# Kernel tuning notes

Measured on AMD Instinct MI355X. Metric: run time of the kernel, lower is better.

Reference implementation:

```python
import jax, jax.numpy as jnp
from jax import lax
import numpy as np

CHUNK = 64      # chunk_size init kwarg
MAX_LOG = 20.0  # clamp bound used in ssd()
DT_BIAS = 0.01
NEG_SLOPE = 0.01  # torch LeakyReLU default


def segsum(a):
    """a: (..., T) -> (..., T, T); ss[i,j] = sum_{k=j+1..i} a[k], -inf above diag."""
    T = a.shape[-1]
    rep = jnp.broadcast_to(a[..., :, None], a.shape + (T,))
    strict_lower = jnp.tril(jnp.ones((T, T), dtype=bool), -1)
    ss = jnp.cumsum(jnp.where(strict_lower, rep, 0.0), axis=-2)
    keep = jnp.tril(jnp.ones((T, T), dtype=bool), 0)
    return jnp.where(keep, ss, -jnp.inf)


def setup_inputs() -> dict:
    key = jax.random.key(0)
    ks = jax.random.split(key, 7)
    T, B, S, F = 4096, 4, 16, 64   # time, batch, spatial heads, in_channels
    N, P, K = 16, 64, 5            # state_dim, head_dim, conv_size
    CH = 2 * N + P + 1             # bc_conv out channels = 97
    return {
        "x": jax.random.normal(ks[0], (T, B, S, F), dtype=jnp.float32),
        "conv_w": jax.random.normal(ks[1], (CH, F, K), dtype=jnp.float32) * 0.05,
        "conv_b": jax.random.normal(ks[2], (CH,), dtype=jnp.float32) * 0.05,
        "pass_w": jax.random.normal(ks[3], (1, F), dtype=jnp.float32) * 0.1,
        "pass_b": jax.random.normal(ks[4], (1,), dtype=jnp.float32) * 0.1,
        "red_w": jax.random.normal(ks[5], (1, P), dtype=jnp.float32) * 0.1,
        "red_b": jax.random.normal(ks[6], (1,), dtype=jnp.float32) * 0.1,
        "dt_param": jnp.zeros((1,), dtype=jnp.float32),  # torch init [0.0]
    }


def _forward(x, conv_w, conv_b, pass_w, pass_b, red_w, red_b, dt_param):
    T, B, S, F = x.shape
    CH, _, K = conv_w.shape
    P = red_w.shape[1]
    N = (CH - P - 1) // 2
    c = T // CHUNK

    # ---- _compute_ssm_params (parallel mode, causal left-pad) ----
    xr = jnp.moveaxis(x.reshape(T, B * S, F), 0, 2)          # (bs, F, T)
    xp = jnp.pad(xr, ((0, 0), (0, 0), (K - 1, 0)))           # left pad context
    bcax = lax.conv_general_dilated(
        xp, conv_w, window_strides=(1,), padding="VALID",
        dimension_numbers=("NCH", "OIH", "NCH")) + conv_b[None, :, None]
    bcax = jax.nn.sigmoid(bcax) + bcax                        # (bs, CH, T)
    bcax = bcax.reshape(B, S, CH, T)
    Bm = bcax[:, :, :N, :]                                    # (b,s,n,t)
    Cm = bcax[:, :, N:2 * N, :]                               # (b,s,n,t)
    A = -jnp.abs(bcax[:, :, 2 * N, :])                        # (b,s,t)
    Xc = bcax[:, :, 2 * N + 1:, :]                            # (b,s,p,t)
    dt = jax.nn.softplus(dt_param)[0] + DT_BIAS
    lAd = dt * A                                              # (b,s,t)
    Bd = Bm * ((jnp.exp(lAd) - 1.0) / (A + 1e-9))[:, :, None, :]
    Dx = x @ pass_w[0] + pass_b[0]                            # (t,b,s) passthrough

    # ---- ssd: chunked Mamba-2 scan ----
    Xb = jnp.moveaxis(Xc, 3, 0).swapaxes(0, 1).reshape(B, c, CHUNK, S, P)
    Bb = jnp.moveaxis(Bd, 3, 0).swapaxes(0, 1).reshape(B, c, CHUNK, S, N)
    Cb = jnp.moveaxis(Cm, 3, 0).swapaxes(0, 1).reshape(B, c, CHUNK, S, N)
    Ab = lAd.reshape(B, S, c, CHUNK)                          # (b,s,c,l)
    A_cumsum = jnp.cumsum(Ab, axis=-1)                        # (b,s,c,l)

    L = jnp.exp(jnp.clip(segsum(Ab), -MAX_LOG, MAX_LOG))      # (b,s,c,l,l)
    Y_diag = jnp.einsum("bclsn,bcmsn,bsclm,bcmsp->bclsp", Cb, Bb, L, Xb)

    decay_states = jnp.exp(jnp.clip(A_cumsum[..., -1:] - A_cumsum, -MAX_LOG, MAX_LOG))
    states = jnp.einsum("bclsn,bscl,bclsp->bcspn", Bb, decay_states, Xb)
    states = jnp.concatenate([jnp.zeros_like(states[:, :1]), states], axis=1)

    A_last = jnp.pad(A_cumsum[..., -1], ((0, 0), (0, 0), (1, 0)))  # (b,s,c+1)
    decay_chunk = jnp.exp(jnp.clip(segsum(A_last), -MAX_LOG, MAX_LOG))
    new_states = jnp.einsum("bszc,bcspn->bzspn", decay_chunk, states)
    states_c = new_states[:, :-1]                             # (b,c,s,p,n)

    state_decay_out = jnp.exp(A_cumsum)                       # (b,s,c,l), no clamp (as in source)
    Y_off = jnp.einsum("bclsn,bcspn,bscl->bclsp", Cb, states_c, state_decay_out)

    Y = (Y_diag + Y_off).reshape(B, T, S, P).swapaxes(0, 1)   # (t,b,s,p)

    # ---- reduce + leaky-relu passthrough ----
    y = Y @ red_w[0] + red_b[0]                               # (t,b,s)
    return y + jnp.where(Dx >= 0, Dx, NEG_SLOPE * Dx)


def reference(x, conv_w, conv_b, pass_w, pass_b, red_w, red_b, dt_param):
    return _forward(x, conv_w, conv_b, pass_w, pass_b, red_w, red_b, dt_param)
```

## Files before the change

kernel.cpp:

```cpp
#include <hip/hip_runtime.h>
#include <hip/hip_bf16.h>
#include <math.h>


#define Tn 4096
#define BSn 64
#define Fn 64
#define CHn 97
#define CHP 112
#define Kn 5
#define Nn 16
#define NCn 64

typedef __attribute__((ext_vector_type(8))) short bf16x8;
typedef __attribute__((ext_vector_type(4))) float f32x4;

static __device__ __forceinline__ unsigned short f2bf(float v) {
    __hip_bfloat16 b = __float2bfloat16(v);
    return *reinterpret_cast<unsigned short*>(&b);
}
static __device__ __forceinline__ float bf2f(unsigned short u) {
    unsigned v = ((unsigned)u) << 16;
    return __builtin_bit_cast(float, v);
}

#define OFF_BD   0
#define OFF_CM   (OFF_BD + 4194304)
#define OFF_LAD  (OFF_CM + 4194304)
#define OFF_XQ   (OFF_LAD + 262144)
#define OFF_DL   (OFF_XQ + 262144)
#define OFF_ACS  (OFF_DL + 262144)
#define OFF_SRED (OFF_ACS + 262144)
#define OFF_CSUM (OFF_SRED + 65536)
#define OFF_SNS  (OFF_CSUM + 4096)
#define OFF_WBH  (OFF_SNS + 65536)
#define OFF_WBL  (OFF_WBH + 17920)

__global__ __launch_bounds__(256) void k_prep(const float* __restrict__ conv_w,
                                              const float* __restrict__ pass_w,
                                              unsigned short* __restrict__ wbh,
                                              unsigned short* __restrict__ wbl) {
    int idx = blockIdx.x * 256 + threadIdx.x;
    if (idx >= Kn * CHP * Fn) return;
    int f = idx & 63;
    int rest = idx >> 6;
    int ch = rest % CHP;
    int k = rest / CHP;
    float w = 0.f;
    if (ch < CHn) w = conv_w[(ch * Fn + f) * Kn + k];
    else if (ch == 97 && k == 4) w = pass_w[f];
    unsigned short hi = f2bf(w);
    wbh[idx] = hi;
    if (ch >= 32 && ch < 48)
        wbl[(k * 16 + (ch - 32)) * 64 + f] = f2bf(w - bf2f(hi));
}

__global__ __launch_bounds__(256) void k_fwd(
    const float* __restrict__ x, const unsigned short* __restrict__ wbh,
    const unsigned short* __restrict__ wbl,
    const float* __restrict__ conv_b, const float* __restrict__ pass_b,
    const float* __restrict__ red_w, const float* __restrict__ red_b,
    const float* __restrict__ dtp,
    float* __restrict__ Cm_t, float* __restrict__ Acs_ws,
    float* __restrict__ yp_ws, float* __restrict__ sred_ws,
    float* __restrict__ csum_ws) {
    const int wgid = blockIdx.x;
    const int seq = wgid >> 3;
    const int bs = seq & 63;
    const int ci = ((seq >> 6) << 3) | (wgid & 7);
    const int tid = threadIdx.x;
    const int wv = tid >> 6, lane = tid & 63;
    const int qd = lane >> 4, n = lane & 15;

    __shared__ alignas(16) unsigned char pool[19584];
    unsigned short* xsb = (unsigned short*)pool;
    unsigned short* xlo = (unsigned short*)(pool + 9792);
    float* B0  = (float*)pool;
    float* Ct  = (float*)(pool + 5120);
    float* pxl = (float*)(pool + 10240);
    float* px2 = (float*)(pool + 11264);
    float* zsh = (float*)(pool + 12288);
    float* dl  = (float*)(pool + 12544);

    const int tB = (wv == 3) ? 6 : wv + 4;
    const unsigned short* pBw = (wv == 2) ? wbl : wbh;
    const int sB = (wv == 2) ? 16 : CHP;
    const int cB = (wv == 2) ? 0 : 16 * tB;
    bf16x8 wA[10], wB[10];
#pragma unroll
    for (int s = 0; s < 10; ++s) {
        const int k = s >> 1, f0 = 32 * (s & 1) + qd * 8;
        wA[s] = *(const bf16x8*)&wbh[((k * CHP + 16 * wv + n) << 6) + f0];
        wB[s] = *(const bf16x8*)&pBw[((k * sB + cB + n) << 6) + f0];
    }

    float4 v[5];
#pragma unroll
    for (int it = 0; it < 5; ++it) {
        int idx = tid + it * 256;
        int tt = idx >> 4, fq = (idx & 15) * 4;
        int t = ci * 64 - 4 + tt;
        v[it] = (idx < 68 * 16 && t >= 0)
                    ? *(const float4*)&x[(t * 64 + bs) * 64 + fq]
                    : make_float4(0.f, 0.f, 0.f, 0.f);
    }
#pragma unroll
    for (int it = 0; it < 5; ++it) {
        int idx = tid + it * 256;
        if (idx < 68 * 16) {
            int tt = idx >> 4, fq = (idx & 15) * 4;
            ushort4 h, lo;
            h.x = f2bf(v[it].x); lo.x = f2bf(v[it].x - bf2f(h.x));
            h.y = f2bf(v[it].y); lo.y = f2bf(v[it].y - bf2f(h.y));
            h.z = f2bf(v[it].z); lo.z = f2bf(v[it].z - bf2f(h.z));
            h.w = f2bf(v[it].w); lo.w = f2bf(v[it].w - bf2f(h.w));
            *(ushort4*)&xsb[tt * 72 + fq] = h;
            *(ushort4*)&xlo[tt * 72 + fq] = lo;
        }
    }
    __syncthreads();

    f32x4 accA[4], accB[4];
#pragma unroll
    for (int rg = 0; rg < 4; ++rg) {
        accA[rg] = (f32x4){0.f, 0.f, 0.f, 0.f};
        accB[rg] = (f32x4){0.f, 0.f, 0.f, 0.f};
    }
    if (wv == 2) {
#pragma unroll
        for (int s = 0; s < 10; ++s) {
            const int k = s >> 1, f0 = 32 * (s & 1) + qd * 8;
#pragma unroll
            for (int rg = 0; rg < 4; ++rg) {
                bf16x8 av = *(const bf16x8*)&xsb[(16 * rg + n + k) * 72 + f0];
                bf16x8 al = *(const bf16x8*)&xlo[(16 * rg + n + k) * 72 + f0];
                accA[rg] = __builtin_amdgcn_mfma_f32_16x16x32_bf16(av, wA[s], accA[rg], 0, 0, 0);
                accA[rg] = __builtin_amdgcn_mfma_f32_16x16x32_bf16(al, wA[s], accA[rg], 0, 0, 0);
                accA[rg] = __builtin_amdgcn_mfma_f32_16x16x32_bf16(av, wB[s], accA[rg], 0, 0, 0);
            }
        }
    } else {
#pragma unroll
        for (int s = 0; s < 10; ++s) {
            const int k = s >> 1, f0 = 32 * (s & 1) + qd * 8;
#pragma unroll
            for (int rg = 0; rg < 4; ++rg) {
                bf16x8 av = *(const bf16x8*)&xsb[(16 * rg + n + k) * 72 + f0];
                accA[rg] = __builtin_amdgcn_mfma_f32_16x16x32_bf16(av, wA[s], accA[rg], 0, 0, 0);
                accB[rg] = __builtin_amdgcn_mfma_f32_16x16x32_bf16(av, wB[s], accB[rg], 0, 0, 0);
            }
        }
    }
    __syncthreads();

    const int cbase = (bs * 64 + ci) * 64;
    float px[4][4];
#pragma unroll
    for (int rg = 0; rg < 4; ++rg)
#pragma unroll
        for (int reg = 0; reg < 4; ++reg) px[rg][reg] = 0.f;

    if (wv == 0) {
        const float cb0 = conv_b[n];
        const float cb4 = conv_b[64 + n], rw4 = red_w[31 + n];
#pragma unroll
        for (int rg = 0; rg < 4; ++rg)
#pragma unroll
            for (int reg = 0; reg < 4; ++reg) {
                int row = 16 * rg + 4 * qd + reg;
                float z0 = accA[rg][reg] + cb0;
                float a0 = z0 + 1.f / (1.f + __expf(-z0));
                accA[rg][reg] = a0;
                B0[row * 20 + n] = a0;
                float z4 = accB[rg][reg] + cb4;
                px[rg][reg] = (z4 + 1.f / (1.f + __expf(-z4))) * rw4;
            }
    } else if (wv == 1) {
        const float cb1 = conv_b[16 + n];
        const float cb5 = conv_b[80 + n], rw5 = red_w[47 + n];
#pragma unroll
        for (int rg = 0; rg < 4; ++rg)
#pragma unroll
            for (int reg = 0; reg < 4; ++reg) {
                int row = 16 * rg + 4 * qd + reg;
                float z1 = accA[rg][reg] + cb1;
                float a1 = z1 + 1.f / (1.f + __expf(-z1));
                Ct[row * 20 + n] = a1;
                Cm_t[(cbase + row) * 16 + n] = a1;
                float z5 = accB[rg][reg] + cb5;
                px[rg][reg] = (z5 + 1.f / (1.f + __expf(-z5))) * rw5;
            }
    } else if (wv == 2) {
        const float cb2 = conv_b[32 + n];
        const float rw2 = (n >= 1) ? red_w[n - 1] : 0.f;
#pragma unroll
        for (int rg = 0; rg < 4; ++rg)
#pragma unroll
            for (int reg = 0; reg < 4; ++reg) {
                int row = 16 * rg + 4 * qd + reg;
                if (n == 0) zsh[row] = accA[rg][reg];
                float z = accA[rg][reg] + cb2;
                px[rg][reg] = (z + 1.f / (1.f + __expf(-z))) * rw2;
            }
    } else {
        const float cb3 = conv_b[48 + n], rw3 = red_w[15 + n];
        const float cb6 = conv_b[96], rw6 = red_w[63];
        const float pb = pass_b[0], rb = red_b[0];
#pragma unroll
        for (int rg = 0; rg < 4; ++rg)
#pragma unroll
            for (int reg = 0; reg < 4; ++reg) {
                int row = 16 * rg + 4 * qd + reg;
                float z3 = accA[rg][reg] + cb3;
                px[rg][reg] = (z3 + 1.f / (1.f + __expf(-z3))) * rw3;
                if (n == 0) {
                    float z6 = accB[rg][reg] + cb6;
                    px[rg][reg] += (z6 + 1.f / (1.f + __expf(-z6))) * rw6;
                }
                if (n == 1) {
                    float Dx = accB[rg][reg] + pb;
                    float DL = (Dx >= 0.f) ? Dx : 0.01f * Dx;
                    dl[row] = DL + rb;
                }
            }
    }
#pragma unroll
    for (int m = 1; m < 16; m <<= 1)
#pragma unroll
        for (int rg = 0; rg < 4; ++rg)
#pragma unroll
            for (int reg = 0; reg < 4; ++reg)
                px[rg][reg] += __shfl_xor(px[rg][reg], m, 64);
    if (n == 0)
#pragma unroll
        for (int rg = 0; rg < 4; ++rg)
#pragma unroll
            for (int reg = 0; reg < 4; ++reg)
                pxl[wv * 64 + 16 * rg + 4 * qd + reg] = px[rg][reg];
    __syncthreads();

    const int l = lane;
    const float dt = log1pf(expf(dtp[0])) + 0.01f;
    float zA = zsh[l] + conv_b[32];
    float aA = zA + 1.f / (1.f + __expf(-zA));
    float An = -fabsf(aA);
    float lAd = dt * An;
    float fac = (__expf(lAd) - 1.f) / (An + 1e-9f);
    float s = lAd;
#pragma unroll
    for (int k = 1; k < 64; k <<= 1) {
        float t = __shfl_up(s, k, 64);
        if (l >= k) s += t;
    }
    const float acs_l = s;
    const float tot = __shfl(s, 63, 64);
    float xq = pxl[0 * 64 + l] + pxl[1 * 64 + l] + pxl[2 * 64 + l] + pxl[3 * 64 + l];
    const float wd = fac * xq;
    const float wsd = wd * __expf(fmaxf(tot - acs_l, -20.f));
    if (wv == 3) {
        Acs_ws[bs * Tn + ci * 64 + l] = acs_l;
        if (l == 0) csum_ws[bs * 64 + ci] = tot;
    }

    const float4 cc0 = *(const float4*)&Ct[l * 20 + 0];
    const float4 cc1 = *(const float4*)&Ct[l * 20 + 4];
    const float4 cc2 = *(const float4*)&Ct[l * 20 + 8];
    const float4 cc3 = *(const float4*)&Ct[l * 20 + 12];
    float part = 0.f;
#pragma unroll
    for (int mm = 0; mm < 16; ++mm) {
        const int m = 16 * wv + mm;
        const float4 b0 = *(const float4*)&B0[m * 20 + 0];
        const float4 b1 = *(const float4*)&B0[m * 20 + 4];
        const float4 b2 = *(const float4*)&B0[m * 20 + 8];
        const float4 b3 = *(const float4*)&B0[m * 20 + 12];
        float g = cc0.x * b0.x + cc0.y * b0.y + cc0.z * b0.z + cc0.w * b0.w +
                  cc1.x * b1.x + cc1.y * b1.y + cc1.z * b1.z + cc1.w * b1.w +
                  cc2.x * b2.x + cc2.y * b2.y + cc2.z * b2.z + cc2.w * b2.w +
                  cc3.x * b3.x + cc3.y * b3.y + cc3.z * b3.z + cc3.w * b3.w;
        float am = __shfl(acs_l, m, 64);
        float wm = __shfl(wd, m, 64);
        float arg = (m <= l) ? fmaxf(acs_l - am, -20.f) : -20.f;
        part += __expf(arg) * g * wm;
    }
    px2[wv * 64 + l] = part;

    if (wv == 0) {
        float sp = 0.f;
#pragma unroll
        for (int rg = 0; rg < 4; ++rg)
#pragma unroll
            for (int reg = 0; reg < 4; ++reg)
                sp += accA[rg][reg] * __shfl(wsd, 16 * rg + 4 * qd + reg, 64);
        sp += __shfl_xor(sp, 16, 64);
        sp += __shfl_xor(sp, 32, 64);
        if (l < 16) sred_ws[(bs * 64 + ci) * 16 + l] = sp;
    }
    __syncthreads();

    if (wv == 0)
        yp_ws[bs * Tn + ci * 64 + l] =
            px2[0 * 64 + l] + px2[1 * 64 + l] + px2[2 * 64 + l] + px2[3 * 64 + l] + dl[l];
}

__global__ __launch_bounds__(256) void k_out(
    const float* __restrict__ Cm_t, const float* __restrict__ Acs_ws,
    const float* __restrict__ sred_ws, const float* __restrict__ csum_ws,
    const float* __restrict__ yp_ws, float* __restrict__ out) {
    const int bs = blockIdx.y;
    const int tid = threadIdx.x;
    const int wv = tid >> 6, l = tid & 63;
    const int ci = blockIdx.x * 4 + wv;
    __shared__ float sn[4][16];
    const int base = bs * Tn + ci * 64;

    const float dexp = __expf(csum_ws[bs * 64 + l]);
#pragma unroll
    for (int j = 0; j < 4; ++j) {
        const int n = 4 * wv + j;
        float s = sred_ws[(bs * 64 + l) * 16 + n];
        float d = dexp;
#pragma unroll
        for (int k = 1; k < 64; k <<= 1) {
            float dp = __shfl_up(d, k, 64);
            float sp = __shfl_up(s, k, 64);
            if (l >= k) {
                s = d * sp + s;
                d = d * dp;
            }
        }
        float se = __shfl_up(s, 1, 64);
        float sns = (l == 0) ? 0.f : se;
        if ((l >> 2) == blockIdx.x) sn[l & 3][n] = sns;
    }

    const float4* crow = (const float4*)&Cm_t[((bs * 64 + ci) * 64 + l) * 16];
    float4 c0 = crow[0], c1 = crow[1], c2 = crow[2], c3 = crow[3];
    float yp = yp_ws[base + l];
    float acl = Acs_ws[base + l];
    __syncthreads();

    const float* s = sn[wv];
    float go = c0.x * s[0] + c0.y * s[1] + c0.z * s[2] + c0.w * s[3] +
               c1.x * s[4] + c1.y * s[5] + c1.z * s[6] + c1.w * s[7] +
               c2.x * s[8] + c2.y * s[9] + c2.z * s[10] + c2.w * s[11] +
               c3.x * s[12] + c3.y * s[13] + c3.z * s[14] + c3.w * s[15];
    out[(ci * 64 + l) * 64 + bs] = yp + __expf(acl) * go;
}

extern "C" void kernel_launch(void* const* d_in, const int* in_sizes, int n_in,
                              void* d_out, int out_size, void* d_ws,
                              size_t ws_size, hipStream_t stream) {
    const float* x = (const float*)d_in[0];
    const float* conv_w = (const float*)d_in[1];
    const float* conv_b = (const float*)d_in[2];
    const float* pass_w = (const float*)d_in[3];
    const float* pass_b = (const float*)d_in[4];
    const float* red_w = (const float*)d_in[5];
    const float* red_b = (const float*)d_in[6];
    const float* dtp = (const float*)d_in[7];
    float* out = (float*)d_out;
    float* W = (float*)d_ws;
    (void)in_sizes; (void)n_in; (void)out_size; (void)ws_size;

    float* Cm_t = W + OFF_CM;
    float* yp_ws = W + OFF_DL;
    float* Acs_ws = W + OFF_ACS;
    float* sred_ws = W + OFF_SRED;
    float* csum_ws = W + OFF_CSUM;
    unsigned short* wbh = (unsigned short*)(W + OFF_WBH);
    unsigned short* wbl = (unsigned short*)(W + OFF_WBL);

    k_prep<<<dim3((Kn * CHP * Fn + 255) / 256), dim3(256), 0, stream>>>(
        conv_w, pass_w, wbh, wbl);
    k_fwd<<<dim3(NCn * BSn), dim3(256), 0, stream>>>(
        x, wbh, wbl, conv_b, pass_b, red_w, red_b, dtp,
        Cm_t, Acs_ws, yp_ws, sred_ws, csum_ws);
    k_out<<<dim3(NCn / 4, BSn), dim3(256), 0, stream>>>(
        Cm_t, Acs_ws, sred_ws, csum_ws, yp_ws, out);
}
```

Baseline: 202.0 us.

## Fuse inter-chunk state scan into forward kernel via decoupled look-back chain

Removes the separate k_out kernel. Each workgroup now takes a ticket from an atomic counter so chunks are processed in order, then waits on a per-sequence flag for the previous chunk's carried state. It combines that state with its own, publishes the result, and writes the final output directly. This drops the workspace round-trips for Cm, Acs, yp and sred and one kernel launch. In exchange it adds a serial dependency chain of 64 chunks per sequence, with spin-wait latency on each link.

```diff
diff --git a/kernel.cpp b/kernel.cpp
--- a/kernel.cpp
+++ b/kernel.cpp
@@ -25,6 +25,9 @@
 }
 
 #define OFF_BD   0
+#define OFF_CHS  OFF_BD
+#define OFF_FLG  (OFF_BD + 65536)
+#define OFF_TKT  (OFF_BD + 69888)
 #define OFF_CM   (OFF_BD + 4194304)
 #define OFF_LAD  (OFF_CM + 4194304)
 #define OFF_XQ   (OFF_LAD + 262144)
@@ -39,8 +42,12 @@
 __global__ __launch_bounds__(256) void k_prep(const float* __restrict__ conv_w,
                                               const float* __restrict__ pass_w,
                                               unsigned short* __restrict__ wbh,
-                                              unsigned short* __restrict__ wbl) {
+                                              unsigned short* __restrict__ wbl,
+                                              int* __restrict__ flags,
+                                              int* __restrict__ ticket) {
     int idx = blockIdx.x * 256 + threadIdx.x;
+    if (idx < NCn * BSn) flags[idx] = 0;
+    if (idx == NCn * BSn) *ticket = 0;
     if (idx >= Kn * CHP * Fn) return;
     int f = idx & 63;
     int rest = idx >> 6;
@@ -61,13 +68,8 @@
     const float* __restrict__ conv_b, const float* __restrict__ pass_b,
     const float* __restrict__ red_w, const float* __restrict__ red_b,
     const float* __restrict__ dtp,
-    float* __restrict__ Cm_t, float* __restrict__ Acs_ws,
-    float* __restrict__ yp_ws, float* __restrict__ sred_ws,
-    float* __restrict__ csum_ws) {
-    const int wgid = blockIdx.x;
-    const int seq = wgid >> 3;
-    const int bs = seq & 63;
-    const int ci = ((seq >> 6) << 3) | (wgid & 7);
+    float* __restrict__ Schain, int* __restrict__ flags,
+    int* __restrict__ ticket, float* __restrict__ out) {
     const int tid = threadIdx.x;
     const int wv = tid >> 6, lane = tid & 63;
     const int qd = lane >> 4, n = lane & 15;
@@ -81,6 +83,12 @@
     float* px2 = (float*)(pool + 11264);
     float* zsh = (float*)(pool + 12288);
     float* dl  = (float*)(pool + 12544);
+    float* sn  = (float*)(pool + 12800);
+    __shared__ int tkt_s;
+
+    if (tid == 0) tkt_s = atomicAdd(ticket, 1);
+    __syncthreads();
+    const int bs = tkt_s & 63, ci = tkt_s >> 6;
 
     const int tB = (wv == 3) ? 6 : wv + 4;
     const unsigned short* pBw = (wv == 2) ? wbl : wbh;
@@ -153,7 +161,6 @@
     }
     __syncthreads();
 
-    const int cbase = (bs * 64 + ci) * 64;
     float px[4][4];
 #pragma unroll
     for (int rg = 0; rg < 4; ++rg)
@@ -184,9 +191,7 @@
             for (int reg = 0; reg < 4; ++reg) {
                 int row = 16 * rg + 4 * qd + reg;
                 float z1 = accA[rg][reg] + cb1;
-                float a1 = z1 + 1.f / (1.f + __expf(-z1));
-                Ct[row * 20 + n] = a1;
-                Cm_t[(cbase + row) * 16 + n] = a1;
+                Ct[row * 20 + n] = z1 + 1.f / (1.f + __expf(-z1));
                 float z5 = accB[rg][reg] + cb5;
                 px[rg][reg] = (z5 + 1.f / (1.f + __expf(-z5))) * rw5;
             }
@@ -249,17 +254,51 @@
     float s = lAd;
 #pragma unroll
     for (int k = 1; k < 64; k <<= 1) {
-        float t = __shfl_up(s, k, 64);
-        if (l >= k) s += t;
+        float t2 = __shfl_up(s, k, 64);
+        if (l >= k) s += t2;
     }
     const float acs_l = s;
     const float tot = __shfl(s, 63, 64);
     float xq = pxl[0 * 64 + l] + pxl[1 * 64 + l] + pxl[2 * 64 + l] + pxl[3 * 64 + l];
     const float wd = fac * xq;
     const float wsd = wd * __expf(fmaxf(tot - acs_l, -20.f));
-    if (wv == 3) {
-        Acs_ws[bs * Tn + ci * 64 + l] = acs_l;
-        if (l == 0) csum_ws[bs * 64 + ci] = tot;
+
+    if (wv == 0) {
+        float sp = 0.f;
+#pragma unroll
+        for (int rg = 0; rg < 4; ++rg)
+#pragma unroll
+            for (int reg = 0; reg < 4; ++reg)
+                sp += accA[rg][reg] * __shfl(wsd, 16 * rg + 4 * qd + reg, 64);
+        sp += __shfl_xor(sp, 16, 64);
+        sp += __shfl_xor(sp, 32, 64);
+        if (lane < 16) {
+            const float dloc = __expf(tot);
+            float nprev = 0.f;
+            if (ci > 0) {
+                int* fp = &flags[bs * 64 + (ci - 1)];
+                long spin = 0;
+                while (__hip_atomic_load(fp, __ATOMIC_ACQUIRE,
+                                         __HIP_MEMORY_SCOPE_AGENT) == 0) {
+                    __builtin_amdgcn_s_sleep(2);
+                    if (++spin > 100000000L) break;
+                }
+                nprev = __hip_atomic_load(
+                    &Schain[(bs * 64 + (ci - 1)) * 16 + lane],
+                    __ATOMIC_RELAXED, __HIP_MEMORY_SCOPE_AGENT);
+            }
+            sn[lane] = nprev;
+            if (ci < NCn - 1) {
+                __hip_atomic_store(&Schain[(bs * 64 + ci) * 16 + lane],
+                                   dloc * nprev + sp, __ATOMIC_RELAXED,
+                                   __HIP_MEMORY_SCOPE_AGENT);
+                __builtin_amdgcn_s_waitcnt(0);
+                if (lane == 0)
+                    __hip_atomic_store(&flags[bs * 64 + ci], 1,
+                                       __ATOMIC_RELEASE,
+                                       __HIP_MEMORY_SCOPE_AGENT);
+            }
+        }
     }
 
     const float4 cc0 = *(const float4*)&Ct[l * 20 + 0];
@@ -284,68 +323,17 @@
         part += __expf(arg) * g * wm;
     }
     px2[wv * 64 + l] = part;
+    __syncthreads();
 
     if (wv == 0) {
-        float sp = 0.f;
-#pragma unroll
-        for (int rg = 0; rg < 4; ++rg)
-#pragma unroll
-            for (int reg = 0; reg < 4; ++reg)
-                sp += accA[rg][reg] * __shfl(wsd, 16 * rg + 4 * qd + reg, 64);
-        sp += __shfl_xor(sp, 16, 64);
-        sp += __shfl_xor(sp, 32, 64);
-        if (l < 16) sred_ws[(bs * 64 + ci) * 16 + l] = sp;
-    }
-    __syncthreads();
-
-    if (wv == 0)
-        yp_ws[bs * Tn + ci * 64 + l] =
-            px2[0 * 64 + l] + px2[1 * 64 + l] + px2[2 * 64 + l] + px2[3 * 64 + l] + dl[l];
-}
-
-__global__ __launch_bounds__(256) void k_out(
-    const float* __restrict__ Cm_t, const float* __restrict__ Acs_ws,
-    const float* __restrict__ sred_ws, const float* __restrict__ csum_ws,
-    const float* __restrict__ yp_ws, float* __restrict__ out) {
-    const int bs = blockIdx.y;
-    const int tid = threadIdx.x;
-    const int wv = tid >> 6, l = tid & 63;
-    const int ci = blockIdx.x * 4 + wv;
-    __shared__ float sn[4][16];
-    const int base = bs * Tn + ci * 64;
-
-    const float dexp = __expf(csum_ws[bs * 64 + l]);
-#pragma unroll
-    for (int j = 0; j < 4; ++j) {
-        const int n = 4 * wv + j;
-        float s = sred_ws[(bs * 64 + l) * 16 + n];
-        float d = dexp;
-#pragma unroll
-        for (int k = 1; k < 64; k <<= 1) {
-            float dp = __shfl_up(d, k, 64);
-            float sp = __shfl_up(s, k, 64);
-            if (l >= k) {
-                s = d * sp + s;
-                d = d * dp;
-            }
-        }
-        float se = __shfl_up(s, 1, 64);
-        float sns = (l == 0) ? 0.f : se;
-        if ((l >> 2) == blockIdx.x) sn[l & 3][n] = sns;
-    }
-
-    const float4* crow = (const float4*)&Cm_t[((bs * 64 + ci) * 64 + l) * 16];
-    float4 c0 = crow[0], c1 = crow[1], c2 = crow[2], c3 = crow[3];
-    float yp = yp_ws[base + l];
-    float acl = Acs_ws[base + l];
-    __syncthreads();
-
-    const float* s = sn[wv];
-    float go = c0.x * s[0] + c0.y * s[1] + c0.z * s[2] + c0.w * s[3] +
-               c1.x * s[4] + c1.y * s[5] + c1.z * s[6] + c1.w * s[7] +
-               c2.x * s[8] + c2.y * s[9] + c2.z * s[10] + c2.w * s[11] +
-               c3.x * s[12] + c3.y * s[13] + c3.z * s[14] + c3.w * s[15];
-    out[(ci * 64 + l) * 64 + bs] = yp + __expf(acl) * go;
+        float go = cc0.x * sn[0] + cc0.y * sn[1] + cc0.z * sn[2] + cc0.w * sn[3] +
+                   cc1.x * sn[4] + cc1.y * sn[5] + cc1.z * sn[6] + cc1.w * sn[7] +
+                   cc2.x * sn[8] + cc2.y * sn[9] + cc2.z * sn[10] + cc2.w * sn[11] +
+                   cc3.x * sn[12] + cc3.y * sn[13] + cc3.z * sn[14] + cc3.w * sn[15];
+        float yv = px2[0 * 64 + l] + px2[1 * 64 + l] + px2[2 * 64 + l] +
+                   px2[3 * 64 + l] + dl[l] + __expf(acs_l) * go;
+        out[(ci * 64 + l) * 64 + bs] = yv;
+    }
 }
 
 extern "C" void kernel_launch(void* const* d_in, const int* in_sizes, int n_in,
@@ -363,19 +351,15 @@
     float* W = (float*)d_ws;
     (void)in_sizes; (void)n_in; (void)out_size; (void)ws_size;
 
-    float* Cm_t = W + OFF_CM;
-    float* yp_ws = W + OFF_DL;
-    float* Acs_ws = W + OFF_ACS;
-    float* sred_ws = W + OFF_SRED;
-    float* csum_ws = W + OFF_CSUM;
+    float* Schain = W + OFF_CHS;
+    int* flags = (int*)(W + OFF_FLG);
+    int* ticket = (int*)(W + OFF_TKT);
     unsigned short* wbh = (unsigned short*)(W + OFF_WBH);
     unsigned short* wbl = (unsigned short*)(W + OFF_WBL);
 
     k_prep<<<dim3((Kn * CHP * Fn + 255) / 256), dim3(256), 0, stream>>>(
-        conv_w, pass_w, wbh, wbl);
+        conv_w, pass_w, wbh, wbl, flags, ticket);
     k_fwd<<<dim3(NCn * BSn), dim3(256), 0, stream>>>(
         x, wbh, wbl, conv_b, pass_b, red_w, red_b, dtp,
-        Cm_t, Acs_ws, yp_ws, sred_ws, csum_ws);
-    k_out<<<dim3(NCn / 4, BSn), dim3(256), 0, stream>>>(
-        Cm_t, Acs_ws, sred_ws, csum_ws, yp_ws, out);
-}
+        Schain, flags, ticket, out);
+}
```

Result: slower. 603.3 us (+198.7%).
